# Kernel optimization log

Measured on AMD Instinct MI355X. Metric: run time of the kernel, lower is better.

## Reference

```python
import jax, jax.numpy as jnp
import numpy as np

NUM_CLASSES = 80
M = 50.0  # MAX_ANOT_ANCHOR_POSITION_DISTANCE
ALPHA = 0.25
GAMMA = 2.0
EPS = 1e-4


def setup_inputs() -> dict:
    key = jax.random.key(0)
    k1, k2, k3, k4, k5 = jax.random.split(key, 5)
    B, N, C, K = 8, 100000, NUM_CLASSES, 32
    classifications = jax.random.uniform(k1, (B, N, C), dtype=jnp.float32,
                                         minval=0.01, maxval=0.99)
    regressions = jax.random.normal(k2, (B, N, 3), dtype=jnp.float32)
    # anchors: x,y in [0,1000), alpha in [0, 2*pi)
    axy = jax.random.uniform(k3, (1, N, 2), dtype=jnp.float32) * 1000.0
    aal = jax.random.uniform(k3, (1, N, 1), dtype=jnp.float32) * 6.2831853
    anchors = jnp.concatenate([axy, aal], axis=-1)
    gxy = jax.random.uniform(k4, (B, K, 2), dtype=jnp.float32) * 1000.0
    gal = jax.random.uniform(k4, (B, K, 1), dtype=jnp.float32) * 6.2831853
    lab = jax.random.randint(k5, (B, K, 1), 0, C).astype(jnp.float32)
    annotations = jnp.concatenate([gxy, gal, lab], axis=-1)
    return {"classifications": classifications, "regressions": regressions,
            "anchors": anchors, "annotations": annotations}


def _per_image(cls_p, reg, anchor, ann):
    # cls_p: [N,C], reg: [N,3], anchor: [N,3], ann: [K,4]
    C = cls_p.shape[1]
    cls_p = jnp.clip(cls_p, EPS, 1.0 - EPS)
    # distance [N,K] = 10*sqrt(dx^2+dy^2) + |dalpha|
    dx = anchor[:, 0:1] - ann[None, :, 0]
    dy = anchor[:, 1:2] - ann[None, :, 1]
    da = jnp.abs(anchor[:, 2:3] - ann[None, :, 2])
    dist = 10.0 * jnp.sqrt(dx * dx + dy * dy) + da
    dmin = jnp.min(dist, axis=1)          # [N]
    amin = jnp.argmin(dist, axis=1)       # [N]
    pos = dmin <= 11.0 * M                # [N]
    neg = dmin >= 13.0 * M                # [N]
    assigned = ann[amin]                  # [N,4]
    labels = assigned[:, 3].astype(jnp.int32)
    onehot = jax.nn.one_hot(labels, C, dtype=jnp.bool_)
    targets = jnp.where((neg | pos)[:, None], 0.0, -1.0)   # [N,C]
    targets = jnp.where(pos[:, None] & onehot, 1.0, targets)
    is_pos_t = targets == 1.0
    alpha_f = jnp.where(is_pos_t, ALPHA, 1.0 - ALPHA)
    focal_w = alpha_f * jnp.where(is_pos_t, 1.0 - cls_p, cls_p) ** GAMMA
    bce = -(targets * jnp.log(cls_p) + (1.0 - targets) * jnp.log(1.0 - cls_p))
    cls_loss = jnp.where(targets != -1.0, focal_w * bce, 0.0)
    num_pos = jnp.sum(pos.astype(jnp.float32))
    cls_l = jnp.sum(cls_loss) / jnp.maximum(num_pos, 1.0)
    tgt = assigned[:, :3] - anchor                     # [N,3]
    diff_xy = jnp.abs(tgt[:, :2] - reg[:, :2])         # [N,2]
    diff_ang = 1.0 - jnp.cos(tgt[:, 2] - reg[:, 2])    # [N]
    lxy = jnp.where(diff_xy <= 1.0 / 9.0,
                    0.5 * 9.0 * diff_xy * diff_xy,
                    diff_xy - 0.5 / 9.0)
    posf = pos.astype(jnp.float32)
    denom = jnp.maximum(num_pos, 1.0)
    reg_l = jnp.sum(lxy * posf[:, None]) / (2.0 * denom) \
          + jnp.sum(diff_ang * posf) / denom
    reg_l = jnp.where(num_pos > 0, reg_l, 0.0)
    return cls_l, reg_l


def reference(classifications, regressions, anchors, annotations):
    anchor = anchors[0]  # [N,3]
    cls_ls, reg_ls = jax.vmap(_per_image, in_axes=(0, 0, None, 0))(
        classifications, regressions, anchor, annotations)
    return (jnp.mean(cls_ls, keepdims=True), jnp.mean(reg_ls, keepdims=True))
```

## Files before the change

kernel.cpp:

```cpp
#include <hip/hip_runtime.h>

#define NUM_CLASSES 80
#define K_ANN 32
#define NF4 (NUM_CLASSES / 4)
#define TILE 448
#define ITER (TILE * NF4 / 256)
#define UNROLL 4
#define PREF 4

typedef float f32x4 __attribute__((ext_vector_type(4)));


__global__ __launch_bounds__(256, 8) void focal_main(
    const float* __restrict__ cls,
    const float* __restrict__ reg,
    const float* __restrict__ anc,
    const float* __restrict__ ann,
    float* __restrict__ ws,
    int N, int nblk)
{
    const int b  = blockIdx.y;
    const int bx = blockIdx.x;
    const int t  = threadIdx.x;
    const int n0 = bx * TILE;
    const bool full = (n0 + TILE <= N);

    __shared__ f32x4  s_pref[PREF * 256];
    __shared__ float4 s_ann4[K_ANN];
    __shared__ float  s_g[TILE];

    if (t < K_ANN)
        s_ann4[t] = ((const float4*)(ann + (long long)b * K_ANN * 4))[t];

    const f32x4* __restrict__ base =
        (const f32x4*)(cls + ((long long)b * N + n0) * NUM_CLASSES);

    if (full) {
        const int wid0 = t >> 6;
        #pragma unroll
        for (int u = 0; u < PREF; ++u)
            __builtin_amdgcn_global_load_lds(
                (const __attribute__((address_space(1))) unsigned int*)&base[u * 256 + t],
                (__attribute__((address_space(3))) unsigned int*)&s_pref[u * 256 + wid0 * 64],
                16, 0, 0);
    }
    __syncthreads();

    float csum = 0.f, npos = 0.f, rxy = 0.f, rang = 0.f;

    {
        const int n1 = n0 + t;
        const int n2 = n0 + 256 + t;
        const bool ok1 = n1 < N;
        const bool ok2 = (t < TILE - 256) && (n2 < N);
        const int m1 = ok1 ? n1 : N - 1;
        const int m2 = ok2 ? n2 : N - 1;
        const float ax1 = anc[m1 * 3 + 0], ay1 = anc[m1 * 3 + 1], aa1 = anc[m1 * 3 + 2];
        const float ax2 = anc[m2 * 3 + 0], ay2 = anc[m2 * 3 + 1], aa2 = anc[m2 * 3 + 2];
        const float r01 = reg[((long long)b * N + m1) * 3 + 0];
        const float r11 = reg[((long long)b * N + m1) * 3 + 1];
        const float r21 = reg[((long long)b * N + m1) * 3 + 2];
        const float r02 = reg[((long long)b * N + m2) * 3 + 0];
        const float r12 = reg[((long long)b * N + m2) * 3 + 1];
        const float r22 = reg[((long long)b * N + m2) * 3 + 2];

        float d1 = 1e30f, d2 = 1e30f;
        int   k1 = 0,     k2 = 0;
        #pragma unroll 4
        for (int k = 0; k < K_ANN; ++k) {
            const float4 a4 = s_ann4[k];
            {
                const float dx = ax1 - a4.x, dy = ay1 - a4.y;
                const float da = fabsf(aa1 - a4.z);
                const float d  = fmaf(10.f, sqrtf(fmaf(dx, dx, dy * dy)), da);
                if (d < d1) { d1 = d; k1 = k; }
            }
            {
                const float dx = ax2 - a4.x, dy = ay2 - a4.y;
                const float da = fabsf(aa2 - a4.z);
                const float d  = fmaf(10.f, sqrtf(fmaf(dx, dx, dy * dy)), da);
                if (d < d2) { d2 = d; k2 = k; }
            }
        }

        #pragma unroll
        for (int r = 0; r < 2; ++r) {
            const bool  ok   = r ? ok2 : ok1;
            const int   n    = r ? n2  : n1;
            const float dmin = r ? d2  : d1;
            const int   kmin = r ? k2  : k1;
            const float ax   = r ? ax2 : ax1;
            const float ay   = r ? ay2 : ay1;
            const float aa   = r ? aa2 : aa1;
            const float rr0  = r ? r02 : r01;
            const float rr1  = r ? r12 : r11;
            const float rr2  = r ? r22 : r21;

            const bool pos = ok && (dmin <= 550.f);
            const bool neg = ok && (dmin >= 650.f);
            if (r == 0 || t < TILE - 256)
                s_g[r * 256 + t] = (pos | neg) ? 0.51986038f : 0.f;

            if (pos) {
                const float4 a4 = s_ann4[kmin];
                const float tx = a4.x - ax, ty = a4.y - ay, tz = a4.z - aa;
                const float dxr = fabsf(tx - rr0);
                const float dyr = fabsf(ty - rr1);
                rxy += ((dxr <= 1.f / 9.f) ? 4.5f * dxr * dxr : dxr - 0.5f / 9.f)
                     + ((dyr <= 1.f / 9.f) ? 4.5f * dyr * dyr : dyr - 0.5f / 9.f);
                rang += 1.f - __cosf(tz - rr2);
                npos += 1.f;

                const int lab = (int)a4.w;
                const float p = cls[((long long)b * N + n) * NUM_CLASSES + lab];
                csum += 0.75f * p * p * __logf(1.f - p)
                      - 0.25f * (1.f - p) * (1.f - p) * __logf(p);
            }
        }
    }
    __syncthreads();

    float acc = 0.f;
    if (full) {
        #pragma unroll
        for (int u = 0; u < PREF; ++u) {
            const unsigned idx = (unsigned)(u * 256 + t);
            const float g = s_g[idx / 20u];
            const f32x4 v = s_pref[idx];
            float s4 = 0.f;
            s4 = fmaf(v.x * v.x, __log2f(1.f - v.x), s4);
            s4 = fmaf(v.y * v.y, __log2f(1.f - v.y), s4);
            s4 = fmaf(v.z * v.z, __log2f(1.f - v.z), s4);
            s4 = fmaf(v.w * v.w, __log2f(1.f - v.w), s4);
            acc = fmaf(g, s4, acc);
        }
        #pragma unroll 1
        for (int i0 = PREF; i0 + UNROLL <= ITER; i0 += UNROLL) {
            unsigned ix[UNROLL];
            float    g [UNROLL];
            f32x4    v [UNROLL];
            #pragma unroll
            for (int u = 0; u < UNROLL; ++u) {
                ix[u] = (unsigned)((i0 + u) * 256 + t);
                g[u]  = s_g[ix[u] / 20u];
            }
            #pragma unroll
            for (int u = 0; u < UNROLL; ++u)
                v[u] = base[(g[u] != 0.f) ? ix[u] : (unsigned)t];
            __builtin_amdgcn_sched_barrier(0);
            #pragma unroll
            for (int u = 0; u < UNROLL; ++u) {
                float s4 = 0.f;
                s4 = fmaf(v[u].x * v[u].x, __log2f(1.f - v[u].x), s4);
                s4 = fmaf(v[u].y * v[u].y, __log2f(1.f - v[u].y), s4);
                s4 = fmaf(v[u].z * v[u].z, __log2f(1.f - v[u].z), s4);
                s4 = fmaf(v[u].w * v[u].w, __log2f(1.f - v[u].w), s4);
                acc = fmaf(g[u], s4, acc);
            }
        }
        #pragma unroll
        for (int i0 = PREF + ((ITER - PREF) / UNROLL) * UNROLL; i0 < ITER; ++i0) {
            const unsigned idx = (unsigned)(i0 * 256 + t);
            const float g = s_g[idx / 20u];
            const f32x4 v = base[(g != 0.f) ? idx : (unsigned)t];
            float s4 = 0.f;
            s4 = fmaf(v.x * v.x, __log2f(1.f - v.x), s4);
            s4 = fmaf(v.y * v.y, __log2f(1.f - v.y), s4);
            s4 = fmaf(v.z * v.z, __log2f(1.f - v.z), s4);
            s4 = fmaf(v.w * v.w, __log2f(1.f - v.w), s4);
            acc = fmaf(g, s4, acc);
        }
    } else {
        const int total4 = (N - n0) * NF4;
        for (int i = t; i < total4; i += 256) {
            const float g = s_g[(unsigned)i / 20u];
            const f32x4 v = base[(g != 0.f) ? i : t];
            float s4 = 0.f;
            s4 = fmaf(v.x * v.x, __log2f(1.f - v.x), s4);
            s4 = fmaf(v.y * v.y, __log2f(1.f - v.y), s4);
            s4 = fmaf(v.z * v.z, __log2f(1.f - v.z), s4);
            s4 = fmaf(v.w * v.w, __log2f(1.f - v.w), s4);
            acc = fmaf(g, s4, acc);
        }
    }
    csum -= acc;

    #pragma unroll
    for (int off = 32; off > 0; off >>= 1) {
        csum += __shfl_down(csum, off);
        npos += __shfl_down(npos, off);
        rxy  += __shfl_down(rxy , off);
        rang += __shfl_down(rang, off);
    }
    __shared__ float s_red[4][4];
    const int wid = t >> 6;
    if ((t & 63) == 0) {
        s_red[wid][0] = csum; s_red[wid][1] = npos;
        s_red[wid][2] = rxy;  s_red[wid][3] = rang;
    }
    __syncthreads();
    if (t == 0) {
        float a0 = 0.f, a1 = 0.f, a2 = 0.f, a3 = 0.f;
        #pragma unroll
        for (int w = 0; w < 4; ++w) {
            a0 += s_red[w][0]; a1 += s_red[w][1];
            a2 += s_red[w][2]; a3 += s_red[w][3];
        }
        float4* slot = (float4*)(ws + ((long long)b * nblk + bx) * 4);
        *slot = make_float4(a0, a1, a2, a3);
    }
}

__global__ __launch_bounds__(512) void focal_final(
    const float* __restrict__ ws, float* __restrict__ out, int B, int nblk)
{
    const int t    = threadIdx.x;
    const int b    = t >> 6;
    const int lane = t & 63;

    float a0 = 0.f, a1 = 0.f, a2 = 0.f, a3 = 0.f;
    if (b < B) {
        for (int i = lane; i < nblk; i += 64) {
            const float4 v = *(const float4*)(ws + ((long long)b * nblk + i) * 4);
            a0 += v.x; a1 += v.y; a2 += v.z; a3 += v.w;
        }
    }
    #pragma unroll
    for (int off = 32; off > 0; off >>= 1) {
        a0 += __shfl_down(a0, off);
        a1 += __shfl_down(a1, off);
        a2 += __shfl_down(a2, off);
        a3 += __shfl_down(a3, off);
    }

    __shared__ float s_cl[8], s_rl[8];
    if (lane == 0 && b < B) {
        const float den = fmaxf(a1, 1.f);
        s_cl[b] = a0 / den;
        const float r = a2 / (2.f * den) + a3 / den;
        s_rl[b] = (a1 > 0.f) ? r : 0.f;
    }
    __syncthreads();
    if (t == 0) {
        float cl = 0.f, rl = 0.f;
        for (int i = 0; i < B; ++i) { cl += s_cl[i]; rl += s_rl[i]; }
        out[0] = cl / (float)B;
        out[1] = rl / (float)B;
    }
}

extern "C" void kernel_launch(void* const* d_in, const int* in_sizes, int n_in,
                              void* d_out, int out_size, void* d_ws, size_t ws_size,
                              hipStream_t stream)
{
    (void)n_in; (void)out_size; (void)ws_size;
    const float* cls = (const float*)d_in[0];
    const float* reg = (const float*)d_in[1];
    const float* anc = (const float*)d_in[2];
    const float* ann = (const float*)d_in[3];
    float* out = (float*)d_out;
    float* ws  = (float*)d_ws;

    const int N = in_sizes[2] / 3;
    const int B = in_sizes[3] / (K_ANN * 4);
    const int nblk = (N + TILE - 1) / TILE;

    dim3 grid(nblk, B);
    focal_main<<<grid, dim3(256), 0, stream>>>(cls, reg, anc, ann, ws, N, nblk);
    focal_final<<<1, dim3(512), 0, stream>>>(ws, out, B, nblk);
}
```

Measured before the change: 51.94 us.

## Fuse final reduction into main kernel via last-block atomic counters

Drops the separate focal_final launch. Each block writes its partial sums and bumps a per-image atomic counter, and the last block for each image reduces that image's partials. A second counter lets the last image-reducer compute the final mean. This removes one kernel launch and its dependency gap, but adds a hipMemsetAsync to reset the counters and some serialized tail work in the last blocks.

```diff
diff --git a/kernel.cpp b/kernel.cpp
--- a/kernel.cpp
+++ b/kernel.cpp
@@ -17,6 +17,7 @@
     const float* __restrict__ anc,
     const float* __restrict__ ann,
     float* __restrict__ ws,
+    float* __restrict__ out,
     int N, int nblk)
 {
     const int b  = blockIdx.y;
@@ -28,6 +29,8 @@
     __shared__ f32x4  s_pref[PREF * 256];
     __shared__ float4 s_ann4[K_ANN];
     __shared__ float  s_g[TILE];
+    __shared__ float  s_red[4][4];
+    __shared__ int    s_last;
 
     if (t < K_ANN)
         s_ann4[t] = ((const float4*)(ann + (long long)b * K_ANN * 4))[t];
@@ -192,13 +195,16 @@
         rxy  += __shfl_down(rxy , off);
         rang += __shfl_down(rang, off);
     }
-    __shared__ float s_red[4][4];
     const int wid = t >> 6;
     if ((t & 63) == 0) {
         s_red[wid][0] = csum; s_red[wid][1] = npos;
         s_red[wid][2] = rxy;  s_red[wid][3] = rang;
     }
     __syncthreads();
+
+    float* const resb = ws + (size_t)gridDim.y * nblk * 4;
+    unsigned* const cnts = (unsigned*)(resb + 16);
+
     if (t == 0) {
         float a0 = 0.f, a1 = 0.f, a2 = 0.f, a3 = 0.f;
         #pragma unroll
@@ -206,46 +212,65 @@
             a0 += s_red[w][0]; a1 += s_red[w][1];
             a2 += s_red[w][2]; a3 += s_red[w][3];
         }
-        float4* slot = (float4*)(ws + ((long long)b * nblk + bx) * 4);
-        *slot = make_float4(a0, a1, a2, a3);
-    }
-}
-
-__global__ __launch_bounds__(512) void focal_final(
-    const float* __restrict__ ws, float* __restrict__ out, int B, int nblk)
-{
-    const int t    = threadIdx.x;
-    const int b    = t >> 6;
-    const int lane = t & 63;
-
-    float a0 = 0.f, a1 = 0.f, a2 = 0.f, a3 = 0.f;
-    if (b < B) {
-        for (int i = lane; i < nblk; i += 64) {
-            const float4 v = *(const float4*)(ws + ((long long)b * nblk + i) * 4);
-            a0 += v.x; a1 += v.y; a2 += v.z; a3 += v.w;
-        }
-    }
-    #pragma unroll
-    for (int off = 32; off > 0; off >>= 1) {
-        a0 += __shfl_down(a0, off);
-        a1 += __shfl_down(a1, off);
-        a2 += __shfl_down(a2, off);
-        a3 += __shfl_down(a3, off);
-    }
-
-    __shared__ float s_cl[8], s_rl[8];
-    if (lane == 0 && b < B) {
-        const float den = fmaxf(a1, 1.f);
-        s_cl[b] = a0 / den;
-        const float r = a2 / (2.f * den) + a3 / den;
-        s_rl[b] = (a1 > 0.f) ? r : 0.f;
-    }
-    __syncthreads();
-    if (t == 0) {
-        float cl = 0.f, rl = 0.f;
-        for (int i = 0; i < B; ++i) { cl += s_cl[i]; rl += s_rl[i]; }
-        out[0] = cl / (float)B;
-        out[1] = rl / (float)B;
+        float* slot = ws + ((long long)b * nblk + bx) * 4;
+        __hip_atomic_store(slot + 0, a0, __ATOMIC_RELAXED, __HIP_MEMORY_SCOPE_AGENT);
+        __hip_atomic_store(slot + 1, a1, __ATOMIC_RELAXED, __HIP_MEMORY_SCOPE_AGENT);
+        __hip_atomic_store(slot + 2, a2, __ATOMIC_RELAXED, __HIP_MEMORY_SCOPE_AGENT);
+        __hip_atomic_store(slot + 3, a3, __ATOMIC_RELAXED, __HIP_MEMORY_SCOPE_AGENT);
+        asm volatile("s_waitcnt vmcnt(0)" ::: "memory");
+        s_last = (atomicAdd(&cnts[b], 1u) == (unsigned)nblk - 1u);
+    }
+    __syncthreads();
+    if (!s_last) return;
+
+    {
+        float a0 = 0.f, a1 = 0.f, a2 = 0.f, a3 = 0.f;
+        for (int i = t; i < nblk; i += 256) {
+            const float* sp = ws + ((long long)b * nblk + i) * 4;
+            a0 += __hip_atomic_load(sp + 0, __ATOMIC_RELAXED, __HIP_MEMORY_SCOPE_AGENT);
+            a1 += __hip_atomic_load(sp + 1, __ATOMIC_RELAXED, __HIP_MEMORY_SCOPE_AGENT);
+            a2 += __hip_atomic_load(sp + 2, __ATOMIC_RELAXED, __HIP_MEMORY_SCOPE_AGENT);
+            a3 += __hip_atomic_load(sp + 3, __ATOMIC_RELAXED, __HIP_MEMORY_SCOPE_AGENT);
+        }
+        #pragma unroll
+        for (int off = 32; off > 0; off >>= 1) {
+            a0 += __shfl_down(a0, off);
+            a1 += __shfl_down(a1, off);
+            a2 += __shfl_down(a2, off);
+            a3 += __shfl_down(a3, off);
+        }
+        if ((t & 63) == 0) {
+            s_red[wid][0] = a0; s_red[wid][1] = a1;
+            s_red[wid][2] = a2; s_red[wid][3] = a3;
+        }
+        __syncthreads();
+        if (t == 0) {
+            float b0 = 0.f, b1 = 0.f, b2 = 0.f, b3 = 0.f;
+            #pragma unroll
+            for (int w = 0; w < 4; ++w) {
+                b0 += s_red[w][0]; b1 += s_red[w][1];
+                b2 += s_red[w][2]; b3 += s_red[w][3];
+            }
+            const float den = fmaxf(b1, 1.f);
+            const float cl = b0 / den;
+            const float rl = (b1 > 0.f) ? (b2 / (2.f * den) + b3 / den) : 0.f;
+            __hip_atomic_store(resb + 2 * b + 0, cl, __ATOMIC_RELAXED, __HIP_MEMORY_SCOPE_AGENT);
+            __hip_atomic_store(resb + 2 * b + 1, rl, __ATOMIC_RELAXED, __HIP_MEMORY_SCOPE_AGENT);
+            asm volatile("s_waitcnt vmcnt(0)" ::: "memory");
+            s_last = (atomicAdd(&cnts[gridDim.y], 1u) == gridDim.y - 1u);
+        }
+        __syncthreads();
+        if (!s_last) return;
+
+        if (t == 0) {
+            float cl = 0.f, rl = 0.f;
+            for (int i = 0; i < (int)gridDim.y; ++i) {
+                cl += __hip_atomic_load(resb + 2 * i + 0, __ATOMIC_RELAXED, __HIP_MEMORY_SCOPE_AGENT);
+                rl += __hip_atomic_load(resb + 2 * i + 1, __ATOMIC_RELAXED, __HIP_MEMORY_SCOPE_AGENT);
+            }
+            out[0] = cl / (float)gridDim.y;
+            out[1] = rl / (float)gridDim.y;
+        }
     }
 }
 
@@ -265,7 +290,9 @@
     const int B = in_sizes[3] / (K_ANN * 4);
     const int nblk = (N + TILE - 1) / TILE;
 
+    hipMemsetAsync((char*)d_ws + ((size_t)B * nblk * 4 + 16) * 4, 0,
+                   (B + 1) * 4, stream);
+
     dim3 grid(nblk, B);
-    focal_main<<<grid, dim3(256), 0, stream>>>(cls, reg, anc, ann, ws, N, nblk);
-    focal_final<<<1, dim3(512), 0, stream>>>(ws, out, B, nblk);
+    focal_main<<<grid, dim3(256), 0, stream>>>(cls, reg, anc, ann, ws, out, N, nblk);
 }
```

Measured after the change: 65.14 us. 25.4% more time.
